# Optimization experiments

Measured on AMD Instinct MI355X. Metric: run time of the kernel, lower is better.

Reference implementation:

```python
import jax, jax.numpy as jnp
import numpy as np

N, F_IN, HID, HEADS, CLASSES, E = 50000, 256, 64, 4, 64, 800000
NEG_SLOPE = 0.2


def _glorot(key, shape):
    fan = shape[0] + shape[-1]
    return jax.random.normal(key, shape, jnp.float32) * jnp.sqrt(2.0 / fan)


def setup_inputs() -> dict:
    key = jax.random.key(0)
    ks = jax.random.split(key, 12)
    x = jax.random.normal(ks[0], (N, F_IN), jnp.float32)
    edge_index = jax.random.randint(ks[1], (2, E), 0, N, jnp.int32)
    d = {"x": x, "edge_index": edge_index}
    dims = [(F_IN, HID), (HEADS * HID, HID), (HEADS * HID, CLASSES)]
    k = 2
    for li, (din, dout) in enumerate(dims, start=1):
        d[f"W{li}"] = _glorot(ks[k], (din, HEADS * dout)); k += 1
        d[f"a_src{li}"] = _glorot(ks[k], (HEADS, dout)); k += 1
        d[f"a_dst{li}"] = _glorot(ks[k], (HEADS, dout)); k += 1
        bdim = HEADS * dout if li < 3 else dout
        d[f"b{li}"] = jnp.zeros((bdim,), jnp.float32)
    return d


def _gat_layer(x, src, dst, W, a_src, a_dst, b, out_dim, concat):
    n = x.shape[0]
    h = (x @ W).reshape(n, HEADS, out_dim)            # [N,H,D]
    al_s = jnp.einsum("nhd,hd->nh", h, a_src)         # [N,H]
    al_d = jnp.einsum("nhd,hd->nh", h, a_dst)
    logits = jax.nn.leaky_relu(al_s[src] + al_d[dst], NEG_SLOPE)  # [E,H]
    # segment softmax over destination nodes (self-loops guarantee non-empty)
    m = jax.ops.segment_max(logits, dst, num_segments=n)
    e = jnp.exp(logits - m[dst])
    denom = jax.ops.segment_sum(e, dst, num_segments=n)
    att = e / denom[dst]                              # [E,H]
    msg = h[src] * att[:, :, None]                    # [E,H,D]
    out = jax.ops.segment_sum(msg, dst, num_segments=n)
    out = out.reshape(n, HEADS * out_dim) if concat else out.mean(axis=1)
    return out + b


def reference(x, edge_index, W1, a_src1, a_dst1, b1, W2, a_src2, a_dst2, b2,
              W3, a_src3, a_dst3, b3):
    loop = jnp.arange(N, dtype=edge_index.dtype)
    src = jnp.concatenate([edge_index[0], loop])
    dst = jnp.concatenate([edge_index[1], loop])
    h = _gat_layer(x, src, dst, W1, a_src1, a_dst1, b1, HID, True)
    h = jax.nn.elu(h)  # dropout is identity in eval mode
    h = _gat_layer(h, src, dst, W2, a_src2, a_dst2, b2, HID, True)
    h = jax.nn.elu(h)
    h = _gat_layer(h, src, dst, W3, a_src3, a_dst3, b3, CLASSES, False)
    return jax.nn.log_softmax(h, axis=-1)
```

## Files before the change

### kernel.cpp

```cpp
#include <hip/hip_runtime.h>
#include <stdint.h>

typedef __bf16 bf16x8 __attribute__((ext_vector_type(8)));
typedef float f32x4 __attribute__((ext_vector_type(4)));
typedef unsigned short u16x8 __attribute__((ext_vector_type(8)));

__device__ __forceinline__ unsigned short f2bf(float f){
  union { float f; unsigned u; } c; c.f = f;
  unsigned u = c.u;
  unsigned r = u + 0x7FFFu + ((u >> 16) & 1u);
  return (unsigned short)(r >> 16);
}

__global__ void k_hist(const int* __restrict__ ei, int E, int Nn, int* __restrict__ counts){
  int total = E + Nn;
  for (int e = blockIdx.x*blockDim.x + threadIdx.x; e < total; e += gridDim.x*blockDim.x){
    int d = (e < E) ? ei[E + e] : (e - E);
    atomicAdd(&counts[d], 1);
  }
}

__global__ __launch_bounds__(1024) void k_scan1(const int* __restrict__ counts, int* __restrict__ rowptr,
                                                int* __restrict__ bsum, int n){
  __shared__ int wsum[17];
  int tid = threadIdx.x, lane = tid & 63, wid = tid >> 6;
  int i = blockIdx.x*1024 + tid;
  int v = (i < n) ? counts[i] : 0;
  int iv = v;
  #pragma unroll
  for (int off = 1; off < 64; off <<= 1){
    int t = __shfl_up(iv, off, 64);
    if (lane >= off) iv += t;
  }
  if (lane == 63) wsum[wid] = iv;
  __syncthreads();
  if (tid == 0){
    int run = 0;
    for (int w = 0; w < 16; ++w){ int t = wsum[w]; wsum[w] = run; run += t; }
    wsum[16] = run;
  }
  __syncthreads();
  if (i < n) rowptr[i + 1] = iv + wsum[wid];
  if (tid == 0) bsum[blockIdx.x] = wsum[16];
}

__global__ __launch_bounds__(1024) void k_scan2(int* __restrict__ bsum, int nb){
  __shared__ int wsum[17];
  int tid = threadIdx.x, lane = tid & 63, wid = tid >> 6;
  int v = (tid < nb) ? bsum[tid] : 0;
  int iv = v;
  #pragma unroll
  for (int off = 1; off < 64; off <<= 1){
    int t = __shfl_up(iv, off, 64);
    if (lane >= off) iv += t;
  }
  if (lane == 63) wsum[wid] = iv;
  __syncthreads();
  if (tid == 0){
    int run = 0;
    for (int w = 0; w < 16; ++w){ int t = wsum[w]; wsum[w] = run; run += t; }
  }
  __syncthreads();
  if (tid < nb) bsum[tid] = iv + wsum[wid] - v;
}

__global__ void k_scan3(int* __restrict__ rowptr, const int* __restrict__ bsum,
                        const int* __restrict__ counts, int* __restrict__ cursor, int n){
  int i = blockIdx.x*blockDim.x + threadIdx.x;
  if (i == 0) rowptr[0] = 0;
  if (i < n){
    int v = rowptr[i + 1] + bsum[i >> 10];
    rowptr[i + 1] = v;
    cursor[i] = v - counts[i];
  }
}

__global__ void k_scatter(const int* __restrict__ ei, int E, int Nn,
                          int* __restrict__ cursor, int* __restrict__ srcs){
  int total = E + Nn;
  for (int e = blockIdx.x*blockDim.x + threadIdx.x; e < total; e += gridDim.x*blockDim.x){
    int s, d;
    if (e < E){ s = ei[e]; d = ei[E + e]; } else { s = d = e - E; }
    int pos = atomicAdd(&cursor[d], 1);
    srcs[pos] = s;
  }
}

__global__ void k_transpose_all(const float* __restrict__ W1, const float* __restrict__ W2,
                                const float* __restrict__ W3, unsigned short* __restrict__ wt1,
                                unsigned short* __restrict__ wt2, unsigned short* __restrict__ wt3){
  int t = blockIdx.x*blockDim.x + threadIdx.x;
  int which = t >> 16, li = t & 65535;
  int k = li >> 8, c = li & 255;
  const float* W = (which == 0) ? W1 : (which == 1) ? W2 : W3;
  unsigned short* Wt = (which == 0) ? wt1 : (which == 1) ? wt2 : wt3;
  Wt[c*256 + k] = f2bf(W[k*256 + c]);
}

template<bool AF32>
__global__ __launch_bounds__(512) void k_gemm3(const void* __restrict__ Av,
                                               const unsigned short* __restrict__ Wt,
                                               const float* __restrict__ asrc,
                                               const float* __restrict__ adst,
                                               unsigned short* __restrict__ H,
                                               float* __restrict__ als,
                                               float* __restrict__ ald,
                                               int Nn, int T, int G){
  __shared__ unsigned short As[64][264];
  int tid = threadIdx.x;
  int wid = tid >> 6, lane = tid & 63;
  int w = wid & 3, rh = wid >> 2;
  int r = lane & 15, kg = lane >> 4;

  const unsigned short* a16 = (const unsigned short*)Av;
  const float*          a32 = (const float*)Av;

  uint4  sreg[4];
  float4 sregf[4][2];

  auto load_tile = [&](int t){
    #pragma unroll
    for (int it = 0; it < 4; ++it){
      int li = it*512 + tid;
      int rr = li >> 5, c16 = li & 31;
      int gr = t*64 + rr; if (gr >= Nn) gr = Nn - 1;
      if (AF32){
        const float* ap = a32 + (size_t)gr*256 + c16*8;
        sregf[it][0] = *reinterpret_cast<const float4*>(ap);
        sregf[it][1] = *reinterpret_cast<const float4*>(ap + 4);
      } else {
        sreg[it] = *reinterpret_cast<const uint4*>(a16 + (size_t)gr*256 + c16*8);
      }
    }
  };
  auto write_lds = [&](){
    #pragma unroll
    for (int it = 0; it < 4; ++it){
      int li = it*512 + tid;
      int rr = li >> 5, c16 = li & 31;
      if (AF32){
        float4 v0 = sregf[it][0], v1 = sregf[it][1];
        union { uint4 q; unsigned short s[8]; } u;
        u.s[0]=f2bf(v0.x); u.s[1]=f2bf(v0.y); u.s[2]=f2bf(v0.z); u.s[3]=f2bf(v0.w);
        u.s[4]=f2bf(v1.x); u.s[5]=f2bf(v1.y); u.s[6]=f2bf(v1.z); u.s[7]=f2bf(v1.w);
        *reinterpret_cast<uint4*>(&As[rr][c16*8]) = u.q;
      } else {
        *reinterpret_cast<uint4*>(&As[rr][c16*8]) = sreg[it];
      }
    }
  };

  float as_c[4], ad_c[4];
  #pragma unroll
  for (int c = 0; c < 4; ++c){
    as_c[c] = asrc[w*64 + c*16 + r];
    ad_c[c] = adst[w*64 + c*16 + r];
  }

  int t = blockIdx.x;
  if (t >= T) return;
  load_tile(t);

  for (;;){
    write_lds();
    __syncthreads();
    int tn = t + G;
    bool more = (tn < T);
    if (more) load_tile(tn);

    f32x4 acc[2][4] = {};
    #pragma unroll
    for (int k0 = 0; k0 < 256; k0 += 32){
      bf16x8 a0 = *reinterpret_cast<const bf16x8*>(&As[rh*32 +      r][kg*8 + k0]);
      bf16x8 a1 = *reinterpret_cast<const bf16x8*>(&As[rh*32 + 16 + r][kg*8 + k0]);
      #pragma unroll
      for (int c = 0; c < 4; ++c){
        bf16x8 bfr = *reinterpret_cast<const bf16x8*>(Wt + (size_t)(w*64 + c*16 + r)*256 + kg*8 + k0);
        acc[0][c] = __builtin_amdgcn_mfma_f32_16x16x32_bf16(a0, bfr, acc[0][c], 0, 0, 0);
        acc[1][c] = __builtin_amdgcn_mfma_f32_16x16x32_bf16(a1, bfr, acc[1][c], 0, 0, 0);
      }
    }

    int rbase = t*64 + rh*32;
    #pragma unroll
    for (int n = 0; n < 2; ++n){
      #pragma unroll
      for (int i = 0; i < 4; ++i){
        int row = rbase + n*16 + kg*4 + i;
        if (row < Nn){
          #pragma unroll
          for (int c = 0; c < 4; ++c)
            H[(size_t)row*256 + w*64 + c*16 + r] = f2bf(acc[n][c][i]);
        }
      }
    }
    #pragma unroll
    for (int n = 0; n < 2; ++n){
      #pragma unroll
      for (int i = 0; i < 4; ++i){
        float ps = acc[n][0][i]*as_c[0] + acc[n][1][i]*as_c[1]
                 + acc[n][2][i]*as_c[2] + acc[n][3][i]*as_c[3];
        float pd = acc[n][0][i]*ad_c[0] + acc[n][1][i]*ad_c[1]
                 + acc[n][2][i]*ad_c[2] + acc[n][3][i]*ad_c[3];
        #pragma unroll
        for (int off = 1; off < 16; off <<= 1){
          ps += __shfl_xor(ps, off, 64);
          pd += __shfl_xor(pd, off, 64);
        }
        int row = rbase + n*16 + kg*4 + i;
        if (r == 0 && row < Nn){
          als[row*4 + w] = ps;
          ald[row*4 + w] = pd;
        }
      }
    }

    if (!more) break;
    __syncthreads();
    t = tn;
  }
}

template<int MODE>
__global__ __launch_bounds__(256) void k_gather4(const unsigned short* __restrict__ Hm,
                          const int* __restrict__ rowptr, const int* __restrict__ srcs,
                          const float* __restrict__ als, const float* __restrict__ ald,
                          const float* __restrict__ bias,
                          unsigned short* __restrict__ actout, float* __restrict__ finalout, int Nn){
  __shared__ float wlds[4][64][4];
  int gid = blockIdx.x*blockDim.x + threadIdx.x;
  int node = gid >> 6, lane = gid & 63;
  if (node >= Nn) return;
  int wv_id = threadIdx.x >> 6;
  int half = lane >> 5;
  int l32  = lane & 31;
  int fbase = l32 * 8;
  int hd = l32 >> 3;
  unsigned voff = (unsigned)(l32 * 16);

  int beg = rowptr[node], deg = rowptr[node + 1] - beg;
  float4 adv = *reinterpret_cast<const float4*>(ald + (size_t)node*4);

  float acc[4][8];
  #pragma unroll
  for (int u = 0; u < 4; ++u)
    #pragma unroll
    for (int i = 0; i < 8; ++i) acc[u][i] = 0.f;
  float sw0 = 0.f, sw1 = 0.f, sw2 = 0.f, sw3 = 0.f;

  const char* Hb = (const char*)Hm;
  const float* wrow = &wlds[wv_id][0][0];

  for (int cb = 0; cb < deg; cb += 64){
    int chunk = min(64, deg - cb);
    bool valid = (lane < chunk);
    int mysrc = valid ? srcs[beg + cb + lane] : 0;

    float4 a = *reinterpret_cast<const float4*>(als + (size_t)mysrc*4);
    float l0 = a.x + adv.x; l0 = l0 > 0.f ? l0 : 0.2f*l0;
    float l1 = a.y + adv.y; l1 = l1 > 0.f ? l1 : 0.2f*l1;
    float l2 = a.z + adv.z; l2 = l2 > 0.f ? l2 : 0.2f*l2;
    float l3 = a.w + adv.w; l3 = l3 > 0.f ? l3 : 0.2f*l3;
    float4 wvv;
    wvv.x = valid ? __expf(l0) : 0.f;
    wvv.y = valid ? __expf(l1) : 0.f;
    wvv.z = valid ? __expf(l2) : 0.f;
    wvv.w = valid ? __expf(l3) : 0.f;
    sw0 += wvv.x; sw1 += wvv.y; sw2 += wvv.z; sw3 += wvv.w;
    *reinterpret_cast<float4*>(&wlds[wv_id][lane][0]) = wvv;
    asm volatile("s_waitcnt lgkmcnt(0)" ::: "memory");
    __builtin_amdgcn_sched_barrier(0);

    for (int e = 0; e < chunk; e += 8){
      #pragma unroll
      for (int u = 0; u < 4; ++u){
        int pe = e + 2*u;
        int sM = __shfl(mysrc, pe + half, 64);
        uint4 hw = *reinterpret_cast<const uint4*>(Hb + (unsigned)sM*512u + voff);
        float wgt = wrow[(unsigned)(pe + half)*4u + (unsigned)hd];
        float h0 = __uint_as_float(hw.x << 16);
        float h1 = __uint_as_float(hw.x & 0xffff0000u);
        float h2 = __uint_as_float(hw.y << 16);
        float h3 = __uint_as_float(hw.y & 0xffff0000u);
        float h4 = __uint_as_float(hw.z << 16);
        float h5 = __uint_as_float(hw.z & 0xffff0000u);
        float h6 = __uint_as_float(hw.w << 16);
        float h7 = __uint_as_float(hw.w & 0xffff0000u);
        acc[u][0] = fmaf(wgt, h0, acc[u][0]);
        acc[u][1] = fmaf(wgt, h1, acc[u][1]);
        acc[u][2] = fmaf(wgt, h2, acc[u][2]);
        acc[u][3] = fmaf(wgt, h3, acc[u][3]);
        acc[u][4] = fmaf(wgt, h4, acc[u][4]);
        acc[u][5] = fmaf(wgt, h5, acc[u][5]);
        acc[u][6] = fmaf(wgt, h6, acc[u][6]);
        acc[u][7] = fmaf(wgt, h7, acc[u][7]);
      }
    }
  }

  #pragma unroll
  for (int off = 1; off < 64; off <<= 1){
    sw0 += __shfl_xor(sw0, off, 64);
    sw1 += __shfl_xor(sw1, off, 64);
    sw2 += __shfl_xor(sw2, off, 64);
    sw3 += __shfl_xor(sw3, off, 64);
  }
  float sden = (hd == 0) ? sw0 : (hd == 1) ? sw1 : (hd == 2) ? sw2 : sw3;
  float inv = 1.f / sden;

  float accf[8];
  #pragma unroll
  for (int i = 0; i < 8; ++i){
    float t = acc[0][i] + acc[1][i] + acc[2][i] + acc[3][i];
    t += __shfl_xor(t, 32, 64);
    accf[i] = t;
  }

  if (MODE == 0){
    if (lane < 32){
      float4 b0 = *reinterpret_cast<const float4*>(bias + fbase);
      float4 b1 = *reinterpret_cast<const float4*>(bias + fbase + 4);
      float o[8];
      o[0] = accf[0]*inv + b0.x; o[1] = accf[1]*inv + b0.y;
      o[2] = accf[2]*inv + b0.z; o[3] = accf[3]*inv + b0.w;
      o[4] = accf[4]*inv + b1.x; o[5] = accf[5]*inv + b1.y;
      o[6] = accf[6]*inv + b1.z; o[7] = accf[7]*inv + b1.w;
      u16x8 pk;
      #pragma unroll
      for (int i = 0; i < 8; ++i){
        float v = o[i];
        v = v > 0.f ? v : __expf(v) - 1.f;
        pk[i] = f2bf(v);
      }
      *reinterpret_cast<u16x8*>(actout + (size_t)node*256 + fbase) = pk;
    }
  } else {
    float v[8];
    #pragma unroll
    for (int i = 0; i < 8; ++i){
      float t = accf[i]*inv;
      t += __shfl_xor(t, 8, 64);
      t += __shfl_xor(t, 16, 64);
      v[i] = t;
    }
    int k = l32 & 7;
    float4 b0 = *reinterpret_cast<const float4*>(bias + k*8);
    float4 b1 = *reinterpret_cast<const float4*>(bias + k*8 + 4);
    v[0] = v[0]*0.25f + b0.x; v[1] = v[1]*0.25f + b0.y;
    v[2] = v[2]*0.25f + b0.z; v[3] = v[3]*0.25f + b0.w;
    v[4] = v[4]*0.25f + b1.x; v[5] = v[5]*0.25f + b1.y;
    v[6] = v[6]*0.25f + b1.z; v[7] = v[7]*0.25f + b1.w;
    float mx = v[0];
    #pragma unroll
    for (int i = 1; i < 8; ++i) mx = fmaxf(mx, v[i]);
    #pragma unroll
    for (int off = 1; off < 8; off <<= 1) mx = fmaxf(mx, __shfl_xor(mx, off, 64));
    float se = 0.f;
    #pragma unroll
    for (int i = 0; i < 8; ++i) se += __expf(v[i] - mx);
    #pragma unroll
    for (int off = 1; off < 8; off <<= 1) se += __shfl_xor(se, off, 64);
    float lse = mx + __logf(se);
    if (lane < 8){
      float4 o0, o1;
      o0.x = v[0]-lse; o0.y = v[1]-lse; o0.z = v[2]-lse; o0.w = v[3]-lse;
      o1.x = v[4]-lse; o1.y = v[5]-lse; o1.z = v[6]-lse; o1.w = v[7]-lse;
      float* dst = finalout + (size_t)node*64 + lane*8;
      *reinterpret_cast<float4*>(dst)     = o0;
      *reinterpret_cast<float4*>(dst + 4) = o1;
    }
  }
}

extern "C" void kernel_launch(void* const* d_in, const int* in_sizes, int n_in,
                              void* d_out, int out_size, void* d_ws, size_t ws_size,
                              hipStream_t stream){
  const float* x     = (const float*)d_in[0];
  const int*   ei    = (const int*)  d_in[1];
  const float* W1    = (const float*)d_in[2];
  const float* asrc1 = (const float*)d_in[3];
  const float* adst1 = (const float*)d_in[4];
  const float* b1    = (const float*)d_in[5];
  const float* W2    = (const float*)d_in[6];
  const float* asrc2 = (const float*)d_in[7];
  const float* adst2 = (const float*)d_in[8];
  const float* b2    = (const float*)d_in[9];
  const float* W3    = (const float*)d_in[10];
  const float* asrc3 = (const float*)d_in[11];
  const float* adst3 = (const float*)d_in[12];
  const float* b3    = (const float*)d_in[13];
  float* out = (float*)d_out;

  int N = in_sizes[0] / 256;
  int E = in_sizes[1] / 2;

  char* p = (char*)d_ws;
  auto carve = [&](size_t bytes){ void* r = (void*)p; p += (bytes + 511) & ~(size_t)511; return r; };
  unsigned short* bufA = (unsigned short*)carve((size_t)N*256*2);
  unsigned short* bufH = (unsigned short*)carve((size_t)N*256*2);
  unsigned short* bufB = (unsigned short*)carve((size_t)N*256*2);
  unsigned short* wt1  = (unsigned short*)carve(256*256*2);
  unsigned short* wt2  = (unsigned short*)carve(256*256*2);
  unsigned short* wt3  = (unsigned short*)carve(256*256*2);
  float* als    = (float*)carve((size_t)N*4*4);
  float* ald    = (float*)carve((size_t)N*4*4);
  int* rowptr   = (int*)carve((size_t)(N+1)*4);
  int* counts   = (int*)carve((size_t)N*4);
  int* cursor   = (int*)carve((size_t)N*4);
  int* bsum     = (int*)carve((size_t)1024*4);
  int* srcs     = (int*)carve((size_t)(E+N)*4);

  hipMemsetAsync(counts, 0, (size_t)N*4, stream);
  k_hist<<<2048, 256, 0, stream>>>(ei, E, N, counts);
  int nb = (N + 1023) / 1024;
  k_scan1<<<nb, 1024, 0, stream>>>(counts, rowptr, bsum, N);
  k_scan2<<<1, 1024, 0, stream>>>(bsum, nb);
  k_scan3<<<(N + 255)/256, 256, 0, stream>>>(rowptr, bsum, counts, cursor, N);
  k_scatter<<<2048, 256, 0, stream>>>(ei, E, N, cursor, srcs);

  k_transpose_all<<<768, 256, 0, stream>>>(W1, W2, W3, wt1, wt2, wt3);

  int T = (N + 63) / 64;
  int G = (T + 1) / 2;
  int nodeblocks = (N*64 + 255)/256;

  k_gemm3<true><<<G, 512, 0, stream>>>(x, wt1, asrc1, adst1, bufH, als, ald, N, T, G);
  k_gather4<0><<<nodeblocks, 256, 0, stream>>>(bufH, rowptr, srcs, als, ald, b1, bufB, nullptr, N);
  k_gemm3<false><<<G, 512, 0, stream>>>(bufB, wt2, asrc2, adst2, bufH, als, ald, N, T, G);
  k_gather4<0><<<nodeblocks, 256, 0, stream>>>(bufH, rowptr, srcs, als, ald, b2, bufA, nullptr, N);
  k_gemm3<false><<<G, 512, 0, stream>>>(bufA, wt3, asrc3, adst3, bufH, als, ald, N, T, G);
  k_gather4<1><<<nodeblocks, 256, 0, stream>>>(bufH, rowptr, srcs, als, ald, b3, nullptr, out, N);
}
```

Baseline: 418.0 us.

## Stage GEMM output through LDS for coalesced stores; batch gather loads with packed FMA

The GEMM epilogue now writes bf16 results into shared memory and then stores full 16-byte rows to global memory. Before, each thread scattered 2-byte stores. The gather kernel issues all NPF row loads before any arithmetic to raise memory-level parallelism. It also accumulates in float2 vectors so the compiler can emit packed FMA. Costs are extra barriers and LDS reuse in the GEMM, and higher register pressure in the gather when NPF is 8.

```diff
diff --git a/kernel.cpp b/kernel.cpp
--- a/kernel.cpp
+++ b/kernel.cpp
@@ -3,6 +3,7 @@
 
 typedef __bf16 bf16x8 __attribute__((ext_vector_type(8)));
 typedef float f32x4 __attribute__((ext_vector_type(4)));
+typedef float f32x2 __attribute__((ext_vector_type(2)));
 typedef unsigned short u16x8 __attribute__((ext_vector_type(8)));
 
 __device__ __forceinline__ unsigned short f2bf(float f){
@@ -10,6 +11,12 @@
   unsigned u = c.u;
   unsigned r = u + 0x7FFFu + ((u >> 16) & 1u);
   return (unsigned short)(r >> 16);
+}
+__device__ __forceinline__ f32x2 bf2x(unsigned p){
+  f32x2 r;
+  r[0] = __uint_as_float(p << 16);
+  r[1] = __uint_as_float(p & 0xffff0000u);
+  return r;
 }
 
 __global__ void k_hist(const int* __restrict__ ei, int E, int Nn, int* __restrict__ counts){
@@ -98,7 +105,7 @@
 }
 
 template<bool AF32>
-__global__ __launch_bounds__(512) void k_gemm3(const void* __restrict__ Av,
+__global__ __launch_bounds__(512) void k_gemm4(const void* __restrict__ Av,
                                                const unsigned short* __restrict__ Wt,
                                                const float* __restrict__ asrc,
                                                const float* __restrict__ adst,
@@ -181,19 +188,6 @@
       }
     }
 
-    int rbase = t*64 + rh*32;
-    #pragma unroll
-    for (int n = 0; n < 2; ++n){
-      #pragma unroll
-      for (int i = 0; i < 4; ++i){
-        int row = rbase + n*16 + kg*4 + i;
-        if (row < Nn){
-          #pragma unroll
-          for (int c = 0; c < 4; ++c)
-            H[(size_t)row*256 + w*64 + c*16 + r] = f2bf(acc[n][c][i]);
-        }
-      }
-    }
     #pragma unroll
     for (int n = 0; n < 2; ++n){
       #pragma unroll
@@ -207,7 +201,7 @@
           ps += __shfl_xor(ps, off, 64);
           pd += __shfl_xor(pd, off, 64);
         }
-        int row = rbase + n*16 + kg*4 + i;
+        int row = t*64 + rh*32 + n*16 + kg*4 + i;
         if (r == 0 && row < Nn){
           als[row*4 + w] = ps;
           ald[row*4 + w] = pd;
@@ -215,14 +209,37 @@
       }
     }
 
+    __syncthreads();
+    #pragma unroll
+    for (int n = 0; n < 2; ++n){
+      #pragma unroll
+      for (int i = 0; i < 4; ++i){
+        int lrow = rh*32 + n*16 + kg*4 + i;
+        #pragma unroll
+        for (int c = 0; c < 4; ++c)
+          As[lrow][w*64 + c*16 + r] = f2bf(acc[n][c][i]);
+      }
+    }
+    __syncthreads();
+    #pragma unroll
+    for (int it = 0; it < 4; ++it){
+      int li = it*512 + tid;
+      int rr = li >> 5, c16 = li & 31;
+      int grow = t*64 + rr;
+      if (grow < Nn){
+        uint4 v = *reinterpret_cast<const uint4*>(&As[rr][c16*8]);
+        *reinterpret_cast<uint4*>(H + (size_t)grow*256 + c16*8) = v;
+      }
+    }
+
     if (!more) break;
     __syncthreads();
     t = tn;
   }
 }
 
-template<int MODE>
-__global__ __launch_bounds__(256) void k_gather4(const unsigned short* __restrict__ Hm,
+template<int MODE, int NPF>
+__global__ __launch_bounds__(256) void k_gather5(const unsigned short* __restrict__ Hm,
                           const int* __restrict__ rowptr, const int* __restrict__ srcs,
                           const float* __restrict__ als, const float* __restrict__ ald,
                           const float* __restrict__ bias,
@@ -241,11 +258,11 @@
   int beg = rowptr[node], deg = rowptr[node + 1] - beg;
   float4 adv = *reinterpret_cast<const float4*>(ald + (size_t)node*4);
 
-  float acc[4][8];
+  f32x2 acc2[4][4];
   #pragma unroll
   for (int u = 0; u < 4; ++u)
     #pragma unroll
-    for (int i = 0; i < 8; ++i) acc[u][i] = 0.f;
+    for (int q = 0; q < 4; ++q) acc2[u][q] = (f32x2){0.f, 0.f};
   float sw0 = 0.f, sw1 = 0.f, sw2 = 0.f, sw3 = 0.f;
 
   const char* Hb = (const char*)Hm;
@@ -271,29 +288,22 @@
     asm volatile("s_waitcnt lgkmcnt(0)" ::: "memory");
     __builtin_amdgcn_sched_barrier(0);
 
-    for (int e = 0; e < chunk; e += 8){
-      #pragma unroll
-      for (int u = 0; u < 4; ++u){
+    for (int e = 0; e < chunk; e += NPF*2){
+      uint4 hw[NPF]; float wgt[NPF];
+      #pragma unroll
+      for (int u = 0; u < NPF; ++u){
         int pe = e + 2*u;
         int sM = __shfl(mysrc, pe + half, 64);
-        uint4 hw = *reinterpret_cast<const uint4*>(Hb + (unsigned)sM*512u + voff);
-        float wgt = wrow[(unsigned)(pe + half)*4u + (unsigned)hd];
-        float h0 = __uint_as_float(hw.x << 16);
-        float h1 = __uint_as_float(hw.x & 0xffff0000u);
-        float h2 = __uint_as_float(hw.y << 16);
-        float h3 = __uint_as_float(hw.y & 0xffff0000u);
-        float h4 = __uint_as_float(hw.z << 16);
-        float h5 = __uint_as_float(hw.z & 0xffff0000u);
-        float h6 = __uint_as_float(hw.w << 16);
-        float h7 = __uint_as_float(hw.w & 0xffff0000u);
-        acc[u][0] = fmaf(wgt, h0, acc[u][0]);
-        acc[u][1] = fmaf(wgt, h1, acc[u][1]);
-        acc[u][2] = fmaf(wgt, h2, acc[u][2]);
-        acc[u][3] = fmaf(wgt, h3, acc[u][3]);
-        acc[u][4] = fmaf(wgt, h4, acc[u][4]);
-        acc[u][5] = fmaf(wgt, h5, acc[u][5]);
-        acc[u][6] = fmaf(wgt, h6, acc[u][6]);
-        acc[u][7] = fmaf(wgt, h7, acc[u][7]);
+        hw[u] = *reinterpret_cast<const uint4*>(Hb + (unsigned)sM*512u + voff);
+        wgt[u] = wrow[(unsigned)(pe + half)*4u + (unsigned)hd];
+      }
+      #pragma unroll
+      for (int u = 0; u < NPF; ++u){
+        f32x2 w2 = {wgt[u], wgt[u]};
+        acc2[u & 3][0] += w2 * bf2x(hw[u].x);
+        acc2[u & 3][1] += w2 * bf2x(hw[u].y);
+        acc2[u & 3][2] += w2 * bf2x(hw[u].z);
+        acc2[u & 3][3] += w2 * bf2x(hw[u].w);
       }
     }
   }
@@ -310,10 +320,13 @@
 
   float accf[8];
   #pragma unroll
-  for (int i = 0; i < 8; ++i){
-    float t = acc[0][i] + acc[1][i] + acc[2][i] + acc[3][i];
-    t += __shfl_xor(t, 32, 64);
-    accf[i] = t;
+  for (int q = 0; q < 4; ++q){
+    f32x2 s2 = acc2[0][q] + acc2[1][q] + acc2[2][q] + acc2[3][q];
+    float t0 = s2[0], t1 = s2[1];
+    t0 += __shfl_xor(t0, 32, 64);
+    t1 += __shfl_xor(t1, 32, 64);
+    accf[2*q]   = t0;
+    accf[2*q+1] = t1;
   }
 
   if (MODE == 0){
@@ -424,10 +437,10 @@
   int G = (T + 1) / 2;
   int nodeblocks = (N*64 + 255)/256;
 
-  k_gemm3<true><<<G, 512, 0, stream>>>(x, wt1, asrc1, adst1, bufH, als, ald, N, T, G);
-  k_gather4<0><<<nodeblocks, 256, 0, stream>>>(bufH, rowptr, srcs, als, ald, b1, bufB, nullptr, N);
-  k_gemm3<false><<<G, 512, 0, stream>>>(bufB, wt2, asrc2, adst2, bufH, als, ald, N, T, G);
-  k_gather4<0><<<nodeblocks, 256, 0, stream>>>(bufH, rowptr, srcs, als, ald, b2, bufA, nullptr, N);
-  k_gemm3<false><<<G, 512, 0, stream>>>(bufA, wt3, asrc3, adst3, bufH, als, ald, N, T, G);
-  k_gather4<1><<<nodeblocks, 256, 0, stream>>>(bufH, rowptr, srcs, als, ald, b3, nullptr, out, N);
-}
+  k_gemm4<true><<<G, 512, 0, stream>>>(x, wt1, asrc1, adst1, bufH, als, ald, N, T, G);
+  k_gather5<0,8><<<nodeblocks, 256, 0, stream>>>(bufH, rowptr, srcs, als, ald, b1, bufB, nullptr, N);
+  k_gemm4<false><<<G, 512, 0, stream>>>(bufB, wt2, asrc2, adst2, bufH, als, ald, N, T, G);
+  k_gather5<0,4><<<nodeblocks, 256, 0, stream>>>(bufH, rowptr, srcs, als, ald, b2, bufA, nullptr, N);
+  k_gemm4<false><<<G, 512, 0, stream>>>(bufA, wt3, asrc3, adst3, bufH, als, ald, N, T, G);
+  k_gather5<1,8><<<nodeblocks, 256, 0, stream>>>(bufH, rowptr, srcs, als, ald, b3, nullptr, out, N);
+}
```

Result: slower. 432.2 us (+3.4%).
